# Optimization experiments

Hardware: AMD Instinct MI355X
Metric: run time of the kernel (lower is better)

## Reference

```python
import jax, jax.numpy as jnp
import numpy as np

B, D_IN, T = 8, 1024, 2048
CODEBOOK_SIZE, CODEBOOK_DIM = 8192, 8
EPS = 1e-12  # F.normalize default eps


def _l2_normalize(x, axis=-1):
    # matches torch F.normalize: x / max(||x||_2, eps)
    n = jnp.sqrt(jnp.sum(x * x, axis=axis, keepdims=True))
    return x / jnp.maximum(n, EPS)


def setup_inputs() -> dict:
    key = jax.random.key(0)
    k_z, k_wi, k_bi, k_wo, k_bo, k_cb = jax.random.split(key, 6)
    z = jax.random.normal(k_z, (B, D_IN, T), dtype=jnp.float32)
    # weight_norm(Conv1d) is a reparameterization; the effective weight is a
    # plain [out, in] matrix for a kernel_size=1 conv.
    w_in = jax.random.normal(k_wi, (CODEBOOK_DIM, D_IN), dtype=jnp.float32) * (1.0 / np.sqrt(D_IN))
    b_in = jax.random.normal(k_bi, (CODEBOOK_DIM,), dtype=jnp.float32) * 0.01
    w_out = jax.random.normal(k_wo, (D_IN, CODEBOOK_DIM), dtype=jnp.float32) * (1.0 / np.sqrt(CODEBOOK_DIM))
    b_out = jax.random.normal(k_bo, (D_IN,), dtype=jnp.float32) * 0.01
    codebook = jax.random.normal(k_cb, (CODEBOOK_SIZE, CODEBOOK_DIM), dtype=jnp.float32)
    return {"z": z, "w_in": w_in, "b_in": b_in, "w_out": w_out, "b_out": b_out, "codebook": codebook}


def reference(z, w_in, b_in, w_out, b_out, codebook):
    b, _, t = z.shape
    # in_project: 1x1 conv == matmul over channel dim
    z_e = jnp.einsum('od,bdt->bot', w_in, z) + b_in[None, :, None]  # [B, cd, T]

    # decode_latents
    enc = z_e.transpose(0, 2, 1).reshape(b * t, CODEBOOK_DIM)  # (b t) d
    enc_n = _l2_normalize(enc, axis=1)
    cb_n = _l2_normalize(codebook, axis=1)
    # dist = ||e||^2 - 2 e @ c^T + ||c||^2  (materializes [B*T, K] as original)
    dist = (jnp.sum(enc_n * enc_n, axis=1, keepdims=True)
            - 2.0 * (enc_n @ cb_n.T)
            + jnp.sum(cb_n * cb_n, axis=1)[None, :])
    indices = jnp.argmax(-dist, axis=1).reshape(b, t)  # [B, T] int
    # decode_code uses the UNnormalized codebook
    z_q = codebook[indices].transpose(0, 2, 1)  # [B, cd, T]

    # straight-through estimator
    z_q_st = z_e + jax.lax.stop_gradient(z_q - z_e)
    out = jnp.einsum('od,bdt->bot', w_out, z_q_st) + b_out[None, :, None]  # [B, D, T]

    commit_loss = jnp.zeros((b,), dtype=z.dtype)
    codebook_loss = jnp.zeros((b,), dtype=z.dtype)
    return (out, commit_loss, codebook_loss, indices, z_e)
```

## Files before the change

### kernel.cpp

```cpp
#include <hip/hip_runtime.h>
#include <math.h>

static constexpr int Bq  = 8;
static constexpr int DIN = 1024;
static constexpr int TTT = 2048;
static constexpr int KCB = 8192;

static constexpr size_t OUT_OFS  = 0;
static constexpr size_t LOSS_OFS = (size_t)Bq * DIN * TTT;
static constexpr size_t IDX_OFS  = LOSS_OFS + 16;
static constexpr size_t ZE_OFS   = IDX_OFS + (size_t)Bq * TTT;

static constexpr size_t WS_CBN  = 0;
static constexpr size_t WS_C2   = 65536;
static constexpr size_t WS_WT   = 73728;
static constexpr size_t WS_ENC  = 81920;
static constexpr size_t WS_PART = 212992;
static constexpr size_t WS_IDXI = WS_PART + (size_t)2 * 32 * 16384;

__global__ __launch_bounds__(256) void k0_prep(
    const float* __restrict__ w_in, const float* __restrict__ codebook,
    float* __restrict__ ws, float* __restrict__ out)
{
  int tid = blockIdx.x * 256 + threadIdx.x;
  if (tid < KCB) {
    const float4* cp = (const float4*)(codebook + (size_t)tid * 8);
    float4 a = cp[0], b = cp[1];
    float v[8] = {a.x, a.y, a.z, a.w, b.x, b.y, b.z, b.w};
    float n2 = 0.f;
#pragma unroll
    for (int o = 0; o < 8; o++) n2 = fmaf(v[o], v[o], n2);
    float dn = fmaxf(sqrtf(n2), 1e-12f);
    float u[8];
    float s2 = 0.f;
#pragma unroll
    for (int o = 0; o < 8; o++) { u[o] = v[o] / dn; s2 = fmaf(u[o], u[o], s2); }
    float4* wp = (float4*)(ws + WS_CBN + (size_t)tid * 8);
    wp[0] = make_float4(u[0], u[1], u[2], u[3]);
    wp[1] = make_float4(u[4], u[5], u[6], u[7]);
    ws[WS_C2 + tid] = s2;
  } else if (tid < KCB + DIN) {
    int d = tid - KCB;
#pragma unroll
    for (int o = 0; o < 8; o++) ws[WS_WT + (size_t)d * 8 + o] = w_in[(size_t)o * DIN + d];
  } else if (tid < KCB + DIN + 16) {
    out[LOSS_OFS + (tid - KCB - DIN)] = 0.f;
  }
}

__global__ __launch_bounds__(512) void k1_proj_in(
    const float* __restrict__ z, const float* __restrict__ b_in,
    float* __restrict__ ws, float* __restrict__ out)
{
  __shared__ __align__(16) float lds[16384];
  int tid = threadIdx.x;
  int bx = blockIdx.x;
  int b = bx >> 5;
  int t0 = (bx & 31) << 6;
  {
    const float4* src = (const float4*)(ws + WS_WT);
    float4* dst = (float4*)lds;
#pragma unroll
    for (int i = 0; i < 4; i++) dst[tid + 512 * i] = src[tid + 512 * i];
  }
  __syncthreads();
  int tt = tid & 15;
  int dg = tid >> 4;
  const float* zb = z + (size_t)b * DIN * TTT + t0 + (tt << 2);
  float4 acc[8];
#pragma unroll
  for (int o = 0; o < 8; o++) acc[o] = make_float4(0.f, 0.f, 0.f, 0.f);
  int dbase = dg << 5;
  const float4* wl = (const float4*)lds;
#pragma unroll 4
  for (int i = 0; i < 32; i++) {
    int d = dbase + i;
    float4 zv = *(const float4*)(zb + (size_t)d * TTT);
    float4 w0 = wl[d * 2 + 0];
    float4 w1 = wl[d * 2 + 1];
#define ACC1(o, wsc)                                    \
    acc[o].x = fmaf(wsc, zv.x, acc[o].x);               \
    acc[o].y = fmaf(wsc, zv.y, acc[o].y);               \
    acc[o].z = fmaf(wsc, zv.z, acc[o].z);               \
    acc[o].w = fmaf(wsc, zv.w, acc[o].w);
    ACC1(0, w0.x) ACC1(1, w0.y) ACC1(2, w0.z) ACC1(3, w0.w)
    ACC1(4, w1.x) ACC1(5, w1.y) ACC1(6, w1.z) ACC1(7, w1.w)
#undef ACC1
  }
  __syncthreads();
  {
    float4* pl = (float4*)lds;
#pragma unroll
    for (int o = 0; o < 8; o++) pl[dg * 128 + o * 16 + tt] = acc[o];
  }
  __syncthreads();
  int o = tid >> 6;
  int t = tid & 63;
  float s = 0.f;
#pragma unroll
  for (int g = 0; g < 32; g++) s += lds[g * 512 + o * 64 + t];
  s += b_in[o];
  out[ZE_OFS + ((size_t)b * 8 + o) * TTT + t0 + t] = s;
  ws[WS_ENC + ((size_t)(b * TTT + t0 + t)) * 8 + o] = s;
}

__global__ __launch_bounds__(256) void k2_scan(float* __restrict__ ws)
{
  __shared__ __align__(16) float scb[256 * 8];
  __shared__ float sc2[256];
  int tid = threadIdx.x;
  int rb = blockIdx.x >> 5;
  int ch = blockIdx.x & 31;
  int k0 = ch << 8;
  {
    const float4* src = (const float4*)(ws + WS_CBN + (size_t)(k0 + tid) * 8);
    float4* dst = (float4*)scb;
    dst[tid * 2] = src[0];
    dst[tid * 2 + 1] = src[1];
    sc2[tid] = ws[WS_C2 + k0 + tid];
  }
  int rbase = (rb << 10) + tid;
  float en[4][8], e2[4], best[4];
  int bidx[4];
#pragma unroll
  for (int j = 0; j < 4; j++) {
    int r = rbase + (j << 8);
    const float4* ep = (const float4*)(ws + WS_ENC + (size_t)r * 8);
    float4 a = ep[0], c = ep[1];
    float n2 = 0.f;
    n2 = fmaf(a.x, a.x, n2); n2 = fmaf(a.y, a.y, n2);
    n2 = fmaf(a.z, a.z, n2); n2 = fmaf(a.w, a.w, n2);
    n2 = fmaf(c.x, c.x, n2); n2 = fmaf(c.y, c.y, n2);
    n2 = fmaf(c.z, c.z, n2); n2 = fmaf(c.w, c.w, n2);
    float dn = fmaxf(sqrtf(n2), 1e-12f);
    en[j][0] = a.x / dn; en[j][1] = a.y / dn; en[j][2] = a.z / dn; en[j][3] = a.w / dn;
    en[j][4] = c.x / dn; en[j][5] = c.y / dn; en[j][6] = c.z / dn; en[j][7] = c.w / dn;
    float s2 = 0.f;
#pragma unroll
    for (int o = 0; o < 8; o++) s2 = fmaf(en[j][o], en[j][o], s2);
    e2[j] = s2;
    best[j] = 3.4e38f;
    bidx[j] = 0;
  }
  __syncthreads();
  const float4* cb4 = (const float4*)scb;
#pragma unroll 2
  for (int k = 0; k < 256; k++) {
    float4 c0 = cb4[k * 2];
    float4 c1 = cb4[k * 2 + 1];
    float cc = sc2[k];
#pragma unroll
    for (int j = 0; j < 4; j++) {
      float dot = 0.f;
      dot = fmaf(en[j][0], c0.x, dot); dot = fmaf(en[j][1], c0.y, dot);
      dot = fmaf(en[j][2], c0.z, dot); dot = fmaf(en[j][3], c0.w, dot);
      dot = fmaf(en[j][4], c1.x, dot); dot = fmaf(en[j][5], c1.y, dot);
      dot = fmaf(en[j][6], c1.z, dot); dot = fmaf(en[j][7], c1.w, dot);
      float dist = fmaf(-2.f, dot, e2[j]) + cc;
      if (dist < best[j]) { best[j] = dist; bidx[j] = k0 + k; }
    }
  }
  float2* part = (float2*)(ws + WS_PART);
#pragma unroll
  for (int j = 0; j < 4; j++) {
    int r = rbase + (j << 8);
    part[(size_t)ch * 16384 + r] = make_float2(best[j], __int_as_float(bidx[j]));
  }
}

__global__ __launch_bounds__(256) void k2b_reduce(float* __restrict__ ws, float* __restrict__ out)
{
  int r = blockIdx.x * 256 + threadIdx.x;
  const float2* part = (const float2*)(ws + WS_PART);
  float best = 3.4e38f;
  int bi = 0;
#pragma unroll 4
  for (int ch = 0; ch < 32; ch++) {
    float2 p = part[(size_t)ch * 16384 + r];
    if (p.x < best) { best = p.x; bi = __float_as_int(p.y); }
  }
  out[IDX_OFS + r] = (float)bi;
  ((int*)(ws + WS_IDXI))[r] = bi;
}

__global__ __launch_bounds__(256) void k3_proj_out(
    const float* __restrict__ codebook, const float* __restrict__ w_out,
    const float* __restrict__ b_out, const float* __restrict__ ws,
    float* __restrict__ out)
{
  int bx = blockIdx.x;
  int b = bx >> 7;
  int th = (bx >> 6) & 1;
  int dt = bx & 63;
  int tid = threadIdx.x;
  int t = (th << 10) + (tid << 2);
  const int* idxp = (const int*)(ws + WS_IDXI);
  int4 id = *(const int4*)(idxp + b * TTT + t);
  const float4* cbp = (const float4*)codebook;
  float4 c00 = cbp[(size_t)id.x * 2], c01 = cbp[(size_t)id.x * 2 + 1];
  float4 c10 = cbp[(size_t)id.y * 2], c11 = cbp[(size_t)id.y * 2 + 1];
  float4 c20 = cbp[(size_t)id.z * 2], c21 = cbp[(size_t)id.z * 2 + 1];
  float4 c30 = cbp[(size_t)id.w * 2], c31 = cbp[(size_t)id.w * 2 + 1];
  int d0 = dt << 4;
#pragma unroll 4
  for (int dd = 0; dd < 16; dd++) {
    int d = d0 + dd;
    const float* wr = w_out + (size_t)d * 8;
    float w0 = wr[0], w1 = wr[1], w2 = wr[2], w3 = wr[3];
    float w4 = wr[4], w5 = wr[5], w6 = wr[6], w7 = wr[7];
    float bb = b_out[d];
#define DOT8(lo, hi)                                                          \
    fmaf(w7, hi.w, fmaf(w6, hi.z, fmaf(w5, hi.y, fmaf(w4, hi.x,              \
    fmaf(w3, lo.w, fmaf(w2, lo.z, fmaf(w1, lo.y, fmaf(w0, lo.x, bb))))))))
    float4 r;
    r.x = DOT8(c00, c01);
    r.y = DOT8(c10, c11);
    r.z = DOT8(c20, c21);
    r.w = DOT8(c30, c31);
#undef DOT8
    *(float4*)(out + OUT_OFS + ((size_t)b * DIN + d) * TTT + t) = r;
  }
}

extern "C" void kernel_launch(void* const* d_in, const int* in_sizes, int n_in,
                              void* d_out, int out_size, void* d_ws, size_t ws_size,
                              hipStream_t stream) {
  const float* z        = (const float*)d_in[0];
  const float* w_in     = (const float*)d_in[1];
  const float* b_in     = (const float*)d_in[2];
  const float* w_out    = (const float*)d_in[3];
  const float* b_out    = (const float*)d_in[4];
  const float* codebook = (const float*)d_in[5];
  float* out = (float*)d_out;
  float* ws  = (float*)d_ws;

  k0_prep<<<dim3(37), dim3(256), 0, stream>>>(w_in, codebook, ws, out);
  k1_proj_in<<<dim3(256), dim3(512), 0, stream>>>(z, b_in, ws, out);
  k2_scan<<<dim3(512), dim3(256), 0, stream>>>(ws);
  k2b_reduce<<<dim3(64), dim3(256), 0, stream>>>(ws, out);
  k3_proj_out<<<dim3(1024), dim3(256), 0, stream>>>(codebook, w_out, b_out, ws, out);
}
```

Baseline: 199.9 us.

## Retile codebook scan to 8 rows per thread and simplify distance arithmetic

The scan kernel now keeps 8 encoded rows per thread and walks 128-codeword chunks, so 64 chunks produce partial results instead of 32. The distance is rewritten as 0.5*||c||^2 minus the dot product. The ||e||^2 term and the -2 scale are dropped because they do not change the argmin, which saves FMAs in the inner loop. The change also raises unroll factors in the projection and reduce loops. In exchange the partial-results buffer and the reduce pass double, and register pressure per thread goes up.

```diff
diff --git a/kernel.cpp b/kernel.cpp
--- a/kernel.cpp
+++ b/kernel.cpp
@@ -5,6 +5,9 @@
 static constexpr int DIN = 1024;
 static constexpr int TTT = 2048;
 static constexpr int KCB = 8192;
+
+static constexpr int NCH = 64;
+static constexpr int CPC = 128;
 
 static constexpr size_t OUT_OFS  = 0;
 static constexpr size_t LOSS_OFS = (size_t)Bq * DIN * TTT;
@@ -16,7 +19,7 @@
 static constexpr size_t WS_WT   = 73728;
 static constexpr size_t WS_ENC  = 81920;
 static constexpr size_t WS_PART = 212992;
-static constexpr size_t WS_IDXI = WS_PART + (size_t)2 * 32 * 16384;
+static constexpr size_t WS_IDXI = WS_PART + (size_t)2 * NCH * 16384;
 
 __global__ __launch_bounds__(256) void k0_prep(
     const float* __restrict__ w_in, const float* __restrict__ codebook,
@@ -38,7 +41,7 @@
     float4* wp = (float4*)(ws + WS_CBN + (size_t)tid * 8);
     wp[0] = make_float4(u[0], u[1], u[2], u[3]);
     wp[1] = make_float4(u[4], u[5], u[6], u[7]);
-    ws[WS_C2 + tid] = s2;
+    ws[WS_C2 + tid] = 0.5f * s2;
   } else if (tid < KCB + DIN) {
     int d = tid - KCB;
 #pragma unroll
@@ -72,7 +75,7 @@
   for (int o = 0; o < 8; o++) acc[o] = make_float4(0.f, 0.f, 0.f, 0.f);
   int dbase = dg << 5;
   const float4* wl = (const float4*)lds;
-#pragma unroll 4
+#pragma unroll 8
   for (int i = 0; i < 32; i++) {
     int d = dbase + i;
     float4 zv = *(const float4*)(zb + (size_t)d * TTT);
@@ -106,66 +109,66 @@
 
 __global__ __launch_bounds__(256) void k2_scan(float* __restrict__ ws)
 {
-  __shared__ __align__(16) float scb[256 * 8];
-  __shared__ float sc2[256];
+  __shared__ __align__(16) float4 scb[CPC * 2];
+  __shared__ float sch[CPC];
   int tid = threadIdx.x;
-  int rb = blockIdx.x >> 5;
-  int ch = blockIdx.x & 31;
-  int k0 = ch << 8;
-  {
+  int rb = blockIdx.x >> 6;
+  int ch = blockIdx.x & 63;
+  int k0 = ch << 7;
+  if (tid < CPC) {
     const float4* src = (const float4*)(ws + WS_CBN + (size_t)(k0 + tid) * 8);
-    float4* dst = (float4*)scb;
-    dst[tid * 2] = src[0];
-    dst[tid * 2 + 1] = src[1];
-    sc2[tid] = ws[WS_C2 + k0 + tid];
-  }
-  int rbase = (rb << 10) + tid;
-  float en[4][8], e2[4], best[4];
-  int bidx[4];
-#pragma unroll
-  for (int j = 0; j < 4; j++) {
-    int r = rbase + (j << 8);
-    const float4* ep = (const float4*)(ws + WS_ENC + (size_t)r * 8);
-    float4 a = ep[0], c = ep[1];
-    float n2 = 0.f;
-    n2 = fmaf(a.x, a.x, n2); n2 = fmaf(a.y, a.y, n2);
-    n2 = fmaf(a.z, a.z, n2); n2 = fmaf(a.w, a.w, n2);
-    n2 = fmaf(c.x, c.x, n2); n2 = fmaf(c.y, c.y, n2);
-    n2 = fmaf(c.z, c.z, n2); n2 = fmaf(c.w, c.w, n2);
-    float dn = fmaxf(sqrtf(n2), 1e-12f);
-    en[j][0] = a.x / dn; en[j][1] = a.y / dn; en[j][2] = a.z / dn; en[j][3] = a.w / dn;
-    en[j][4] = c.x / dn; en[j][5] = c.y / dn; en[j][6] = c.z / dn; en[j][7] = c.w / dn;
-    float s2 = 0.f;
-#pragma unroll
-    for (int o = 0; o < 8; o++) s2 = fmaf(en[j][o], en[j][o], s2);
-    e2[j] = s2;
-    best[j] = 3.4e38f;
-    bidx[j] = 0;
-  }
-  __syncthreads();
-  const float4* cb4 = (const float4*)scb;
-#pragma unroll 2
-  for (int k = 0; k < 256; k++) {
-    float4 c0 = cb4[k * 2];
-    float4 c1 = cb4[k * 2 + 1];
-    float cc = sc2[k];
-#pragma unroll
-    for (int j = 0; j < 4; j++) {
-      float dot = 0.f;
-      dot = fmaf(en[j][0], c0.x, dot); dot = fmaf(en[j][1], c0.y, dot);
-      dot = fmaf(en[j][2], c0.z, dot); dot = fmaf(en[j][3], c0.w, dot);
-      dot = fmaf(en[j][4], c1.x, dot); dot = fmaf(en[j][5], c1.y, dot);
-      dot = fmaf(en[j][6], c1.z, dot); dot = fmaf(en[j][7], c1.w, dot);
-      float dist = fmaf(-2.f, dot, e2[j]) + cc;
-      if (dist < best[j]) { best[j] = dist; bidx[j] = k0 + k; }
-    }
+    scb[tid * 2]     = src[0];
+    scb[tid * 2 + 1] = src[1];
+    sch[tid] = ws[WS_C2 + k0 + tid];
+  }
+  int rbase = (rb << 11) + tid;
+
+#define DECL_ROW(j) float4 m##j##a, m##j##b; float b##j = 3.4e38f; int i##j = 0;
+  DECL_ROW(0) DECL_ROW(1) DECL_ROW(2) DECL_ROW(3)
+  DECL_ROW(4) DECL_ROW(5) DECL_ROW(6) DECL_ROW(7)
+#undef DECL_ROW
+
+#define LOAD_ROW(j) {                                                         \
+    int r = rbase + (j << 8);                                                 \
+    const float4* ep = (const float4*)(ws + WS_ENC + (size_t)r * 8);          \
+    float4 a = ep[0], c = ep[1];                                              \
+    float n2 = 0.f;                                                           \
+    n2 = fmaf(a.x, a.x, n2); n2 = fmaf(a.y, a.y, n2);                         \
+    n2 = fmaf(a.z, a.z, n2); n2 = fmaf(a.w, a.w, n2);                         \
+    n2 = fmaf(c.x, c.x, n2); n2 = fmaf(c.y, c.y, n2);                         \
+    n2 = fmaf(c.z, c.z, n2); n2 = fmaf(c.w, c.w, n2);                         \
+    float dn = fmaxf(sqrtf(n2), 1e-12f);                                      \
+    m##j##a.x = -(a.x / dn); m##j##a.y = -(a.y / dn);                         \
+    m##j##a.z = -(a.z / dn); m##j##a.w = -(a.w / dn);                         \
+    m##j##b.x = -(c.x / dn); m##j##b.y = -(c.y / dn);                         \
+    m##j##b.z = -(c.z / dn); m##j##b.w = -(c.w / dn); }
+  LOAD_ROW(0) LOAD_ROW(1) LOAD_ROW(2) LOAD_ROW(3)
+  LOAD_ROW(4) LOAD_ROW(5) LOAD_ROW(6) LOAD_ROW(7)
+#undef LOAD_ROW
+
+  __syncthreads();
+#pragma unroll 4
+  for (int k = 0; k < CPC; k++) {
+    float4 c0 = scb[2 * k];
+    float4 c1 = scb[2 * k + 1];
+    float cc = sch[k];
+    int kk = k0 + k;
+#define STEP(j) {                                                             \
+    float s = cc;                                                             \
+    s = fmaf(m##j##a.x, c0.x, s); s = fmaf(m##j##a.y, c0.y, s);               \
+    s = fmaf(m##j##a.z, c0.z, s); s = fmaf(m##j##a.w, c0.w, s);               \
+    s = fmaf(m##j##b.x, c1.x, s); s = fmaf(m##j##b.y, c1.y, s);               \
+    s = fmaf(m##j##b.z, c1.z, s); s = fmaf(m##j##b.w, c1.w, s);               \
+    if (s < b##j) { b##j = s; i##j = kk; } }
+    STEP(0) STEP(1) STEP(2) STEP(3) STEP(4) STEP(5) STEP(6) STEP(7)
+#undef STEP
   }
   float2* part = (float2*)(ws + WS_PART);
-#pragma unroll
-  for (int j = 0; j < 4; j++) {
-    int r = rbase + (j << 8);
-    part[(size_t)ch * 16384 + r] = make_float2(best[j], __int_as_float(bidx[j]));
-  }
+#define STORE_ROW(j) \
+  part[(size_t)ch * 16384 + rbase + (j << 8)] = make_float2(b##j, __int_as_float(i##j));
+  STORE_ROW(0) STORE_ROW(1) STORE_ROW(2) STORE_ROW(3)
+  STORE_ROW(4) STORE_ROW(5) STORE_ROW(6) STORE_ROW(7)
+#undef STORE_ROW
 }
 
 __global__ __launch_bounds__(256) void k2b_reduce(float* __restrict__ ws, float* __restrict__ out)
@@ -174,8 +177,8 @@
   const float2* part = (const float2*)(ws + WS_PART);
   float best = 3.4e38f;
   int bi = 0;
-#pragma unroll 4
-  for (int ch = 0; ch < 32; ch++) {
+#pragma unroll 8
+  for (int ch = 0; ch < NCH; ch++) {
     float2 p = part[(size_t)ch * 16384 + r];
     if (p.x < best) { best = p.x; bi = __float_as_int(p.y); }
   }
```

Result: no change. 196.1 us (-1.9%).
